# Optimization experiments

Hardware: AMD Instinct MI355X
Metric: run time of the kernel (lower is better)

The kernel has to match this reference:

```python
import jax, jax.numpy as jnp
import numpy as np

EPS = 1e-5

def mvn(x):
    # x: [B, C, H, W]; per-(B,C) mean/std over spatial dims, torch unbiased var
    B, C, H, W = x.shape
    xf = x.reshape(B, C, H * W)
    mean = jnp.mean(xf, axis=2)
    var = jnp.var(xf, axis=2, ddof=1) + EPS
    std = jnp.sqrt(var)
    return (x - mean[:, :, None, None]) / std[:, :, None, None]

def conv1x1(x, w, b):
    # x: [B, Cin, H, W], w: [Cout, Cin], b: [Cout]
    return jnp.einsum('bchw,oc->bohw', x, w) + b[None, :, None, None]

def setup_inputs() -> dict:
    key = jax.random.key(0)
    ks = jax.random.split(key, 10)
    B, V, QK, H, W = 4, 512, 512, 64, 64
    d = {
        'c_x':  jax.random.normal(ks[0], (B, V, H, W), jnp.float32),
        's_x':  jax.random.normal(ks[1], (B, V, H, W), jnp.float32),
        'c_1x': jax.random.normal(ks[2], (B, QK, H, W), jnp.float32),
        's_1x': jax.random.normal(ks[3], (B, QK, H, W), jnp.float32),
        'f_w': jax.random.normal(ks[4], (QK, QK), jnp.float32) * (1.0 / np.sqrt(QK)),
        'f_b': jax.random.normal(ks[5], (QK,), jnp.float32) * 0.01,
        'g_w': jax.random.normal(ks[6], (QK, QK), jnp.float32) * (1.0 / np.sqrt(QK)),
        'g_b': jax.random.normal(ks[7], (QK,), jnp.float32) * 0.01,
        'h_w': jax.random.normal(ks[8], (V, V), jnp.float32) * (1.0 / np.sqrt(V)),
        'h_b': jax.random.normal(ks[9], (V,), jnp.float32) * 0.01,
    }
    return d

def reference(c_x, s_x, c_1x, s_1x, f_w, f_b, g_w, g_b, h_w, h_b):
    B, V, H, W = c_x.shape
    QK = c_1x.shape[1]
    Lq = H * W
    Lk = s_1x.shape[2] * s_1x.shape[3]
    # Q: [B, Lq, QK], K: [B, QK, Lk], V_: [B, Lk, V]
    Q = conv1x1(mvn(c_1x), f_w, f_b).reshape(B, QK, Lq).transpose(0, 2, 1)
    K = conv1x1(mvn(s_1x), g_w, g_b).reshape(B, QK, Lk)
    V_ = conv1x1(s_x, h_w, h_b).reshape(B, V, Lk).transpose(0, 2, 1)
    A = jax.nn.softmax(jnp.einsum('bqc,bck->bqk', Q, K), axis=-1)  # [B, Lq, Lk]
    M = jnp.einsum('bqk,bkv->bqv', A, V_)                          # weighted mean
    Var = jnp.einsum('bqk,bkv->bqv', A, V_ * V_) - M * M           # weighted var
    S = jnp.sqrt(jnp.clip(Var, 0.0, None))
    M = M.transpose(0, 2, 1).reshape(c_x.shape)
    S = S.transpose(0, 2, 1).reshape(c_x.shape)
    return S * mvn(c_x) + M
```

## Files before the change

### kernel.cpp

```cpp
#include <hip/hip_runtime.h>
#include <math.h>

typedef __attribute__((ext_vector_type(8))) short short8;
typedef __attribute__((ext_vector_type(4))) float f32x4;
typedef __attribute__((ext_vector_type(4))) unsigned short u16x4;

#define DEVINL static __device__ __forceinline__
#define MFMA  __builtin_amdgcn_mfma_f32_16x16x32_bf16
#define MFMAH __builtin_amdgcn_mfma_f32_16x16x32_f16

DEVINL unsigned short f2bf(float f){
  union { float f; unsigned u; } v; v.f = f;
  unsigned r = v.u + 0x7FFFu + ((v.u >> 16) & 1u);
  return (unsigned short)(r >> 16);
}
DEVINL float bf2f(unsigned short h){
  union { unsigned u; float f; } v; v.u = ((unsigned)h) << 16;
  return v.f;
}
DEVINL unsigned short f2h(float f){
  union { _Float16 h; unsigned short u; } c; c.h = (_Float16)f;
  return c.u;
}
DEVINL void gload16(const void* g, void* l){
  __builtin_amdgcn_global_load_lds(
      (const __attribute__((address_space(1))) void*)g,
      (__attribute__((address_space(3))) void*)l, 16, 0, 0);
}

__global__ void rowstats_k(const float* __restrict__ x,
                           float* __restrict__ mean, float* __restrict__ rstd){
  int row = blockIdx.x;
  const float4* p = (const float4*)(x + (long)row * 4096);
  float s = 0.f, ss = 0.f;
  for (int i = threadIdx.x; i < 1024; i += 256){
    float4 v = p[i];
    s  += v.x + v.y + v.z + v.w;
    ss += v.x*v.x + v.y*v.y + v.z*v.z + v.w*v.w;
  }
  for (int o = 32; o > 0; o >>= 1){ s += __shfl_down(s, o); ss += __shfl_down(ss, o); }
  __shared__ float ls[4], lss[4];
  int wv = threadIdx.x >> 6;
  if ((threadIdx.x & 63) == 0){ ls[wv] = s; lss[wv] = ss; }
  __syncthreads();
  if (threadIdx.x == 0){
    s = ls[0]+ls[1]+ls[2]+ls[3]; ss = lss[0]+lss[1]+lss[2]+lss[3];
    float m = s * (1.f/4096.f);
    float var = (ss - s*m) * (1.f/4095.f);
    mean[row] = m;
    rstd[row] = 1.f / sqrtf(var + 1e-5f);
  }
}

__global__ void foldw2_k(const float* __restrict__ fw, const float* __restrict__ fb,
                         const float* __restrict__ mQ, const float* __restrict__ rQ,
                         unsigned short* __restrict__ Wfh, unsigned short* __restrict__ Wfl,
                         float* __restrict__ bF,
                         const float* __restrict__ gw, const float* __restrict__ gb,
                         const float* __restrict__ mK, const float* __restrict__ rK,
                         unsigned short* __restrict__ Wgh, unsigned short* __restrict__ Wgl,
                         float* __restrict__ bG){
  int o = blockIdx.x;
  int g = blockIdx.y;
  const float* w    = g ? gw : fw;
  const float* bias = g ? gb : fb;
  const float* mean = g ? mK : mQ;
  const float* rstd = g ? rK : rQ;
  unsigned short* wh = g ? Wgh : Wfh;
  unsigned short* wl = g ? Wgl : Wfl;
  float* biasp = g ? bG : bF;
  const float* wr = w + (long)o * 512;
  float part = 0.f;
  for (int c = threadIdx.x; c < 512; c += 256){
    float wv = wr[c] * rstd[c];
    unsigned short h = f2bf(wv);
    wh[(o<<9)+c] = h;
    wl[(o<<9)+c] = f2bf(wv - bf2f(h));
    part += wv * mean[c];
  }
  __shared__ float red[256];
  red[threadIdx.x] = part; __syncthreads();
  for (int st = 128; st > 0; st >>= 1){
    if (threadIdx.x < st) red[threadIdx.x] += red[threadIdx.x + st];
    __syncthreads();
  }
  if (threadIdx.x == 0) biasp[o] = bias[o] - red[0];
}

__global__ void wsplit_k(const float* __restrict__ w,
                         unsigned short* __restrict__ wh, unsigned short* __restrict__ wl){
  int i = blockIdx.x * 256 + threadIdx.x;
  float v = w[i];
  unsigned short h = f2bf(v);
  wh[i] = h; wl[i] = f2bf(v - bf2f(h));
}

__global__ __launch_bounds__(512) void conv3qk_k(
    const float* __restrict__ X0, const float* __restrict__ X1,
    const unsigned short* __restrict__ Wh0, const unsigned short* __restrict__ Wl0,
    const unsigned short* __restrict__ Wh1, const unsigned short* __restrict__ Wl1,
    const float* __restrict__ b0, const float* __restrict__ b1,
    unsigned short* __restrict__ of0, unsigned short* __restrict__ of1)
{
  int ob = blockIdx.y, lb = blockIdx.x, z = blockIdx.z;
  const float* X = z ? X1 : X0;
  const unsigned short* Wh = z ? Wh1 : Wh0;
  const unsigned short* Wl = z ? Wl1 : Wl0;
  const float* biasp = z ? b1 : b0;
  unsigned short* of = z ? of1 : of0;

  __shared__ __align__(16) char csm[36864];
  typedef unsigned short (*XT)[64][72];
  XT Xh = (XT)csm;
  XT Xl = (XT)(csm + 18432);

  int tid = threadIdx.x, w = tid >> 6, lane = tid & 63, lr = lane & 15, lg = lane >> 4;
  const unsigned short* WhB = Wh + (long)(ob*128 + w*16) * 512;
  const unsigned short* WlB = Wl + (long)(ob*128 + w*16) * 512;
  int sl = tid & 63, scg = tid >> 6;
  const float* Xg = X + (long)(scg*8)*4096 + lb*64 + sl;

  f32x4 acc[4] = {};
  float fA[8], fB[8];
  short8 wA0, wA1, wA2, wA3, wB0, wB1, wB2, wB3;

#define CV_XLOAD(F, CB) { _Pragma("unroll") for (int j=0;j<8;++j) F[j] = Xg[(long)((CB)*64 + j)*4096]; }
#define CV_XWRITE(BUF, F) { short8 hv, lv; _Pragma("unroll") for (int j=0;j<8;++j){ \
    unsigned short h_ = f2bf(F[j]); hv[j] = (short)h_; lv[j] = (short)f2bf(F[j] - bf2f(h_)); } \
    *(short8*)&Xh[BUF][sl][scg*8] = hv; *(short8*)&Xl[BUF][sl][scg*8] = lv; }
#define CV_WLOAD(W0,W1,W2,W3, CB) { \
    W0 = *(const short8*)(WhB + (long)lr*512 + (CB)*64 + lg*8); \
    W1 = *(const short8*)(WhB + (long)lr*512 + (CB)*64 + 32 + lg*8); \
    W2 = *(const short8*)(WlB + (long)lr*512 + (CB)*64 + lg*8); \
    W3 = *(const short8*)(WlB + (long)lr*512 + (CB)*64 + 32 + lg*8); }
#define CV_COMPUTE(BUF, W0,W1,W2,W3) { \
    _Pragma("unroll") for (int ct=0;ct<4;++ct){ \
      short8 bh = *(const short8*)&Xh[BUF][ct*16+lr][lg*8]; \
      short8 bl = *(const short8*)&Xl[BUF][ct*16+lr][lg*8]; \
      acc[ct] = MFMA(W0, bh, acc[ct], 0,0,0); \
      acc[ct] = MFMA(W2, bh, acc[ct], 0,0,0); \
      acc[ct] = MFMA(W0, bl, acc[ct], 0,0,0); } \
    _Pragma("unroll") for (int ct=0;ct<4;++ct){ \
      short8 bh = *(const short8*)&Xh[BUF][ct*16+lr][32+lg*8]; \
      short8 bl = *(const short8*)&Xl[BUF][ct*16+lr][32+lg*8]; \
      acc[ct] = MFMA(W1, bh, acc[ct], 0,0,0); \
      acc[ct] = MFMA(W3, bh, acc[ct], 0,0,0); \
      acc[ct] = MFMA(W1, bl, acc[ct], 0,0,0); } }

  CV_XLOAD(fA, 0); CV_XWRITE(0, fA);
  CV_XLOAD(fA, 1);
  CV_WLOAD(wA0,wA1,wA2,wA3, 0);
  __syncthreads();
  for (int cb = 0; cb < 8; cb += 2){
    if (cb+2 < 8) CV_XLOAD(fB, cb+2);
    CV_WLOAD(wB0,wB1,wB2,wB3, cb+1);
    CV_COMPUTE(0, wA0,wA1,wA2,wA3);
    CV_XWRITE(1, fA);
    __syncthreads();
    if (cb+3 < 8) CV_XLOAD(fA, cb+3);
    if (cb+2 < 8) CV_WLOAD(wA0,wA1,wA2,wA3, cb+2);
    CV_COMPUTE(1, wB0,wB1,wB2,wB3);
    if (cb+2 < 8) CV_XWRITE(0, fB);
    __syncthreads();
  }

  int o4 = ob*128 + w*16 + lg*4;
  float bv[4];
  #pragma unroll
  for (int r = 0; r < 4; ++r) bv[r] = biasp[o4 + r];
  #pragma unroll
  for (int ct = 0; ct < 4; ++ct){
    u16x4 ph;
    #pragma unroll
    for (int r = 0; r < 4; ++r) ph[r] = f2h(acc[ct][r] + bv[r]);
    long base = ((long)(lb*64 + ct*16 + lr)) * 512 + o4;
    *(u16x4*)(of + base) = ph;
  }
}

__global__ __launch_bounds__(512) void conv3v_k(
    const float* __restrict__ X,
    const unsigned short* __restrict__ Wh, const unsigned short* __restrict__ Wl,
    const float* __restrict__ biasp,
    unsigned short* __restrict__ oh,
    unsigned short* __restrict__ o2h, unsigned short* __restrict__ o2l)
{
  int ob = blockIdx.y, lb = blockIdx.x;
  __shared__ __align__(16) char csm[36864];
  typedef unsigned short (*XT)[64][72];
  XT Xh = (XT)csm;
  XT Xl = (XT)(csm + 18432);

  int tid = threadIdx.x, w = tid >> 6, lane = tid & 63, lr = lane & 15, lg = lane >> 4;
  const unsigned short* WhB = Wh + (long)(ob*128 + w*16) * 512;
  const unsigned short* WlB = Wl + (long)(ob*128 + w*16) * 512;
  int sl = tid & 63, scg = tid >> 6;
  const float* Xg = X + (long)(scg*8)*4096 + lb*64 + sl;

  f32x4 acc[4] = {};
  float fA[8], fB[8];
  short8 wA0, wA1, wA2, wA3, wB0, wB1, wB2, wB3;

  CV_XLOAD(fA, 0); CV_XWRITE(0, fA);
  CV_XLOAD(fA, 1);
  CV_WLOAD(wA0,wA1,wA2,wA3, 0);
  __syncthreads();
  for (int cb = 0; cb < 8; cb += 2){
    if (cb+2 < 8) CV_XLOAD(fB, cb+2);
    CV_WLOAD(wB0,wB1,wB2,wB3, cb+1);
    CV_COMPUTE(0, wA0,wA1,wA2,wA3);
    CV_XWRITE(1, fA);
    __syncthreads();
    if (cb+3 < 8) CV_XLOAD(fA, cb+3);
    if (cb+2 < 8) CV_WLOAD(wA0,wA1,wA2,wA3, cb+2);
    CV_COMPUTE(1, wB0,wB1,wB2,wB3);
    if (cb+2 < 8) CV_XWRITE(0, fB);
    __syncthreads();
  }

  int o4 = ob*128 + w*16 + lg*4;
  float bv[4];
  #pragma unroll
  for (int r = 0; r < 4; ++r) bv[r] = biasp[o4 + r];
  unsigned short sh_[16], s2h_[16], s2l_[16];
  #pragma unroll
  for (int ct = 0; ct < 4; ++ct)
    #pragma unroll
    for (int r = 0; r < 4; ++r){
      float y = acc[ct][r] + bv[r];
      unsigned short h = f2bf(y);
      float vhf = bf2f(h);
      float v2 = vhf * vhf;
      unsigned short h2 = f2bf(v2);
      unsigned short l2 = f2bf(v2 - bf2f(h2));
      sh_[ct*4+r] = h; s2h_[ct*4+r] = h2; s2l_[ct*4+r] = l2;
    }
  unsigned short* T = (unsigned short*)csm;
#define CV_STORE(ARR, DST) { \
    __syncthreads(); \
    _Pragma("unroll") for (int ct=0;ct<4;++ct) \
      _Pragma("unroll") for (int r=0;r<4;++r) \
        T[(w*16+lg*4+r)*72 + ct*16+lr] = ARR[ct*4+r]; \
    __syncthreads(); \
    _Pragma("unroll") for (int s_=0;s_<2;++s_){ \
      int slot = tid + s_*512; int row = slot>>3, ch=(slot&7)*8; \
      *(short8*)(DST + (long)(ob*128+row)*4096 + lb*64 + ch) = *(const short8*)&T[row*72+ch]; } }
  CV_STORE(sh_,  oh);
  CV_STORE(s2h_, o2h);
  CV_STORE(s2l_, o2l);
#undef CV_STORE
#undef CV_XLOAD
#undef CV_XWRITE
#undef CV_WLOAD
#undef CV_COMPUTE
}

__global__ __launch_bounds__(512, 4) void sgemm1h_k(
    const unsigned short* __restrict__ Qf, const unsigned short* __restrict__ Kf,
    float* __restrict__ S, int qbase)
{
  int bx = blockIdx.x, by = blockIdx.y;
  int q0g = qbase + bx*128, k0 = by*128;
  __shared__ unsigned short Qs[128][64], Ks[128][64];
  int tid = threadIdx.x, w = tid >> 6, lane = tid & 63, lr = lane & 15, lg = lane >> 4;
  int wr = w & 1, wc = w >> 1;
  int srow = tid >> 3, sch = (tid & 7)*8;
  int swu = ((tid & 7) ^ (srow & 7)) * 8;
  int lr7 = lr & 7;
  short8 qr0, qr1, kr0, kr1;
  f32x4 acc[4][2] = {};

#define SG_LOAD(CB) { long c0_ = (long)(CB)*64 + sch; \
    qr0 = *(const short8*)(Qf + (long)(q0g + srow)*512 + c0_); \
    qr1 = *(const short8*)(Qf + (long)(q0g + srow + 64)*512 + c0_); \
    kr0 = *(const short8*)(Kf + (long)(k0 + srow)*512 + c0_); \
    kr1 = *(const short8*)(Kf + (long)(k0 + srow + 64)*512 + c0_); }
#define SG_WRITE { \
    *(short8*)&Qs[srow][swu] = qr0; *(short8*)&Qs[srow + 64][swu] = qr1; \
    *(short8*)&Ks[srow][swu] = kr0; *(short8*)&Ks[srow + 64][swu] = kr1; }

  SG_LOAD(0); SG_WRITE;
  __syncthreads();
  for (int cb = 0; cb < 8; ++cb){
    if (cb < 7) SG_LOAD(cb+1);
    #pragma unroll
    for (int kk = 0; kk < 2; ++kk){
      int un = ((kk*4 + lg) ^ lr7) * 8;
      short8 bh[2];
      #pragma unroll
      for (int bs = 0; bs < 2; ++bs)
        bh[bs] = *(const short8*)(&Ks[wc*32 + bs*16 + lr][un]);
      #pragma unroll
      for (int as = 0; as < 4; ++as){
        short8 ah = *(const short8*)(&Qs[wr*64 + as*16 + lr][un]);
        #pragma unroll
        for (int bs = 0; bs < 2; ++bs)
          acc[as][bs] = MFMAH(ah, bh[bs], acc[as][bs], 0,0,0);
      }
    }
    __syncthreads();
    if (cb < 7){ SG_WRITE; __syncthreads(); }
  }
#undef SG_LOAD
#undef SG_WRITE
  #pragma unroll
  for (int as = 0; as < 4; ++as){
    #pragma unroll
    for (int bs = 0; bs < 2; ++bs){
      int q = bx*128 + wr*64 + as*16 + lg*4;
      int k = k0 + wc*32 + bs*16 + lr;
      float* Sp = S + (long)q*4096 + k;
      #pragma unroll
      for (int r = 0; r < 4; ++r) Sp[(long)r*4096] = acc[as][bs][r];
    }
  }
}

__global__ __launch_bounds__(256) void softmax_k(const float* __restrict__ S,
                                                 unsigned short* __restrict__ Pb, long pitch,
                                                 int row0, float* __restrict__ inv2){
  int row = blockIdx.x;
  const float* Sr = S + (long)row * 4096;
  int t = threadIdx.x;
  f32x4 v[4];
  #pragma unroll
  for (int i = 0; i < 4; ++i) v[i] = *(const f32x4*)(Sr + t*4 + i*1024);
  float mx = v[0][0];
  #pragma unroll
  for (int i = 0; i < 4; ++i)
    #pragma unroll
    for (int j = 0; j < 4; ++j) mx = fmaxf(mx, v[i][j]);
  #pragma unroll
  for (int o = 32; o > 0; o >>= 1) mx = fmaxf(mx, __shfl_xor(mx, o));
  __shared__ float red[4];
  int wid = t >> 6;
  if ((t & 63) == 0) red[wid] = mx;
  __syncthreads();
  mx = fmaxf(fmaxf(red[0], red[1]), fmaxf(red[2], red[3]));
  __syncthreads();
  float p[16]; float d = 0.f;
  #pragma unroll
  for (int i = 0; i < 4; ++i)
    #pragma unroll
    for (int j = 0; j < 4; ++j){ float e = expf(v[i][j] - mx); p[i*4+j] = e; d += e; }
  #pragma unroll
  for (int o = 32; o > 0; o >>= 1) d += __shfl_xor(d, o);
  if ((t & 63) == 0) red[wid] = d;
  __syncthreads();
  d = red[0] + red[1] + red[2] + red[3];
  __syncthreads();
  float invd = 1.f / d;
  unsigned short pb[16]; float d2 = 0.f;
  #pragma unroll
  for (int i = 0; i < 16; ++i){ pb[i] = f2bf(p[i] * invd); d2 += bf2f(pb[i]); }
  #pragma unroll
  for (int o = 32; o > 0; o >>= 1) d2 += __shfl_xor(d2, o);
  if ((t & 63) == 0) red[wid] = d2;
  __syncthreads();
  if (t == 0) inv2[row0 + row] = 1.f / (red[0]+red[1]+red[2]+red[3]);
  unsigned short* Pr = Pb + (long)(row0 + row) * pitch;
  #pragma unroll
  for (int i = 0; i < 4; ++i){
    u16x4 pk;
    #pragma unroll
    for (int j = 0; j < 4; ++j) pk[j] = pb[i*4+j];
    *(u16x4*)(Pr + t*4 + i*1024) = pk;
  }
}

__global__ __launch_bounds__(256, 2) void pv2_k(
    const unsigned short* __restrict__ P, long ppitch,
    const unsigned short* __restrict__ vh,
    const unsigned short* __restrict__ v2h, const unsigned short* __restrict__ v2l,
    const float* __restrict__ inv2,
    const float* __restrict__ cx, const float* __restrict__ mcx, const float* __restrict__ rcx,
    float* __restrict__ outb, int qP_base, int qG_base)
{
  __shared__ __align__(16) char smem[65536];
  typedef unsigned short (*PlT)[64][64];
  typedef unsigned short (*VlT)[3][64][64];
  PlT Pl = (PlT)smem;
  VlT Vl = (VlT)(smem + 16384);
  float* R = (float*)smem;

  int tid = threadIdx.x;
  int l = tid & 63, w = tid >> 6;
  int wq = w >> 1, wv = w & 1;
  int lr = l & 15, lg = l >> 4;
  int qP0 = qP_base + blockIdx.x*64, qG0 = qG_base + blockIdx.x*64;
  int vc0 = blockIdx.y*64;

  int r8_ = l >> 3, c8 = (l & 7)*8;
  int srcc = c8 ^ (r8_*8);
  const unsigned short* gsrc;
  long rs8;
  unsigned short *l0, *l1;
  if (w == 0){
    gsrc = P + (long)(qP0 + r8_)*ppitch + srcc;
    rs8 = (long)8*ppitch;
    l0 = &Pl[0][0][0]; l1 = &Pl[1][0][0];
  } else {
    const unsigned short* va = (w==1 ? vh : w==2 ? v2h : v2l);
    gsrc = va + (long)(vc0 + r8_)*4096 + srcc;
    rs8 = (long)8*4096;
    l0 = &Vl[0][w-1][0][0]; l1 = &Vl[1][w-1][0][0];
  }

  f32x4 accM[2][2] = {}, acc2[2][2] = {};

#define PV_STAGE(LB, TT) { long ko_ = (long)(TT)*64; \
    _Pragma("unroll") for (int j = 0; j < 8; ++j) \
      gload16(gsrc + j*rs8 + ko_, LB + j*512); }
#define PV_COMPUTE(BUF) { \
    _Pragma("unroll") for (int kk = 0; kk < 2; ++kk){ \
      int un = ((kk*4 + lg) ^ (lr & 7)) * 8; \
      short8 fh[2], f2h[2], f2l[2]; \
      _Pragma("unroll") for (int bs = 0; bs < 2; ++bs){ \
        int vrow = wv*32 + bs*16 + lr; \
        fh[bs]  = *(const short8*)(&Vl[BUF][0][vrow][un]); \
        f2h[bs] = *(const short8*)(&Vl[BUF][1][vrow][un]); \
        f2l[bs] = *(const short8*)(&Vl[BUF][2][vrow][un]); } \
      _Pragma("unroll") for (int aq = 0; aq < 2; ++aq){ \
        short8 pa = *(const short8*)(&Pl[BUF][wq*32 + aq*16 + lr][un]); \
        _Pragma("unroll") for (int bs = 0; bs < 2; ++bs){ \
          accM[aq][bs] = MFMA(pa, fh[bs],  accM[aq][bs], 0,0,0); \
          acc2[aq][bs] = MFMA(pa, f2h[bs], acc2[aq][bs], 0,0,0); \
          acc2[aq][bs] = MFMA(pa, f2l[bs], acc2[aq][bs], 0,0,0); } } } }

  PV_STAGE(l0, 0);
  __syncthreads();
  for (int t = 0; t < 64; ++t){
    unsigned short* nb = (t & 1) ? l0 : l1;
    if (t < 63) PV_STAGE(nb, t+1);
    int buf = t & 1;
    PV_COMPUTE(buf);
    __syncthreads();
  }
#undef PV_STAGE
#undef PV_COMPUTE

  float* Tm = R;
  #pragma unroll
  for (int aq = 0; aq < 2; ++aq)
    #pragma unroll
    for (int bs = 0; bs < 2; ++bs){
      int vcl = wv*32 + bs*16 + lr;
      int ql  = wq*32 + aq*16 + lg*4;
      #pragma unroll
      for (int r = 0; r < 4; ++r) Tm[vcl*68 + ql + r] = accM[aq][bs][r];
    }
  __syncthreads();
  f32x4 Mv[4];
  #pragma unroll
  for (int p = 0; p < 4; ++p){
    int chunk = tid + p*256;
    int row = chunk >> 4, c4 = (chunk & 15)*4;
    Mv[p] = *(const f32x4*)&Tm[row*68 + c4];
  }
  __syncthreads();
  #pragma unroll
  for (int aq = 0; aq < 2; ++aq)
    #pragma unroll
    for (int bs = 0; bs < 2; ++bs){
      int vcl = wv*32 + bs*16 + lr;
      int ql  = wq*32 + aq*16 + lg*4;
      #pragma unroll
      for (int r = 0; r < 4; ++r) Tm[vcl*68 + ql + r] = acc2[aq][bs][r];
    }
  __syncthreads();
  #pragma unroll
  for (int p = 0; p < 4; ++p){
    int chunk = tid + p*256;
    int row = chunk >> 4, c4 = (chunk & 15)*4;
    float mu = mcx[vc0 + row], rs = rcx[vc0 + row];
    f32x4 t2 = *(const f32x4*)&Tm[row*68 + c4];
    f32x4 iv = *(const f32x4*)&inv2[qP0 + c4];
    f32x4 cv = *(const f32x4*)&cx[(long)(vc0+row)*4096 + qG0 + c4];
    f32x4 ov;
    #pragma unroll
    for (int j = 0; j < 4; ++j){
      float M = Mv[p][j]*iv[j], M2 = t2[j]*iv[j];
      float var = M2 - M*M;
      float sd = sqrtf(fmaxf(var, 0.f));
      ov[j] = sd*(cv[j]-mu)*rs + M;
    }
    *(f32x4*)&outb[(long)(vc0+row)*4096 + qG0 + c4] = ov;
  }
}

extern "C" void kernel_launch(void* const* d_in, const int* in_sizes, int n_in,
                              void* d_out, int out_size, void* d_ws, size_t ws_size,
                              hipStream_t stream){
  const float* c_x  = (const float*)d_in[0];
  const float* s_x  = (const float*)d_in[1];
  const float* c_1x = (const float*)d_in[2];
  const float* s_1x = (const float*)d_in[3];
  const float* f_w  = (const float*)d_in[4];
  const float* f_b  = (const float*)d_in[5];
  const float* g_w  = (const float*)d_in[6];
  const float* g_b  = (const float*)d_in[7];
  const float* h_w  = (const float*)d_in[8];
  const float* h_b  = (const float*)d_in[9];
  float* out = (float*)d_out;

  char* ws = (char*)d_ws;
  size_t off = 0;
  auto alloc = [&](size_t bytes)->void*{
    void* p = ws + off; off += (bytes + 255) & ~(size_t)255; return p;
  };
  float* meanQ = (float*)alloc(2048*4); float* rstdQ = (float*)alloc(2048*4);
  float* meanK = (float*)alloc(2048*4); float* rstdK = (float*)alloc(2048*4);
  float* meanC = (float*)alloc(2048*4); float* rstdC = (float*)alloc(2048*4);
  float* biasF = (float*)alloc(512*4);  float* biasG = (float*)alloc(512*4);
  unsigned short* Wfh = (unsigned short*)alloc((size_t)512*512*2);
  unsigned short* Wfl = (unsigned short*)alloc((size_t)512*512*2);
  unsigned short* Wgh = (unsigned short*)alloc((size_t)512*512*2);
  unsigned short* Wgl = (unsigned short*)alloc((size_t)512*512*2);
  unsigned short* Whh = (unsigned short*)alloc((size_t)512*512*2);
  unsigned short* Whl = (unsigned short*)alloc((size_t)512*512*2);
  unsigned short* Qf = (unsigned short*)alloc((size_t)4096*512*2);
  unsigned short* Kf = (unsigned short*)alloc((size_t)4096*512*2);
  unsigned short* vh  = (unsigned short*)alloc((size_t)512*4096*2);
  unsigned short* v2h = (unsigned short*)alloc((size_t)512*4096*2);
  unsigned short* v2l = (unsigned short*)alloc((size_t)512*4096*2);
  float* S    = (float*)alloc((size_t)2048*4096*4);
  float* inv2 = (float*)alloc(4096*4);

  size_t pbytes = (size_t)4096*4096*2;
  bool bigP = (off + pbytes + 256 <= ws_size);
  unsigned short* Pb; long ppitch;
  if (bigP){ Pb = (unsigned short*)alloc(pbytes); ppitch = 4096; }
  else     { Pb = (unsigned short*)S;             ppitch = 8192; }

  rowstats_k<<<2048, 256, 0, stream>>>(c_1x, meanQ, rstdQ);
  rowstats_k<<<2048, 256, 0, stream>>>(s_1x, meanK, rstdK);
  rowstats_k<<<2048, 256, 0, stream>>>(c_x,  meanC, rstdC);
  wsplit_k<<<1024, 256, 0, stream>>>(h_w, Whh, Whl);

  for (int b = 0; b < 4; ++b){
    long xoff = (long)b * 512 * 4096;
    foldw2_k<<<dim3(512,2), 256, 0, stream>>>(f_w, f_b, meanQ + b*512, rstdQ + b*512, Wfh, Wfl, biasF,
                                              g_w, g_b, meanK + b*512, rstdK + b*512, Wgh, Wgl, biasG);
    conv3qk_k<<<dim3(64,4,2), 512, 0, stream>>>(c_1x + xoff, s_1x + xoff,
                                                Wfh, Wfl, Wgh, Wgl, biasF, biasG,
                                                Qf, Kf);
    conv3v_k<<<dim3(64,4), 512, 0, stream>>>(s_x + xoff, Whh, Whl, h_b, vh, v2h, v2l);
    if (bigP){
      for (int ch = 0; ch < 2; ++ch){
        int qbase = ch * 2048;
        sgemm1h_k<<<dim3(16,32), 512, 0, stream>>>(Qf, Kf, S, qbase);
        softmax_k<<<2048, 256, 0, stream>>>(S, Pb, 4096, qbase, inv2);
      }
      pv2_k<<<dim3(64,8), 256, 0, stream>>>(Pb, 4096, vh, v2h, v2l, inv2,
                                            c_x + xoff, meanC + b*512, rstdC + b*512,
                                            out + xoff, 0, 0);
    } else {
      for (int ch = 0; ch < 2; ++ch){
        int qbase = ch * 2048;
        sgemm1h_k<<<dim3(16,32), 512, 0, stream>>>(Qf, Kf, S, qbase);
        softmax_k<<<2048, 256, 0, stream>>>(S, Pb, 8192, 0, inv2);
        pv2_k<<<dim3(32,8), 256, 0, stream>>>(Pb, 8192, vh, v2h, v2l, inv2,
                                              c_x + xoff, meanC + b*512, rstdC + b*512,
                                              out + xoff, 0, qbase);
      }
    }
  }
}
```

Before: 635.1 us.

## Store attention scores in fp16 and softmax in place over full query range

The score GEMM now writes fp16 scores instead of fp32, and softmax overwrites that same buffer with bf16 probabilities. This halves score traffic and drops the separate probability buffer. With the smaller buffer, all 4096 queries run in one pass, collapsing the two-chunk launch sequence into single sgemm/softmax/pv launches per batch. The cost is precision: logits are rounded to fp16 before exp, which may hurt accuracy or overflow for large scores.

Result: faster. 575.4 us (-9.4%).

```diff
diff --git a/kernel.cpp b/kernel.cpp
--- a/kernel.cpp
+++ b/kernel.cpp
@@ -21,6 +21,10 @@
 DEVINL unsigned short f2h(float f){
   union { _Float16 h; unsigned short u; } c; c.h = (_Float16)f;
   return c.u;
+}
+DEVINL float h2f(unsigned short u){
+  union { unsigned short u; _Float16 h; } c; c.u = u;
+  return (float)c.h;
 }
 DEVINL void gload16(const void* g, void* l){
   __builtin_amdgcn_global_load_lds(
@@ -257,10 +261,10 @@
 
 __global__ __launch_bounds__(512, 4) void sgemm1h_k(
     const unsigned short* __restrict__ Qf, const unsigned short* __restrict__ Kf,
-    float* __restrict__ S, int qbase)
+    unsigned short* __restrict__ S)
 {
   int bx = blockIdx.x, by = blockIdx.y;
-  int q0g = qbase + bx*128, k0 = by*128;
+  int q0g = bx*128, k0 = by*128;
   __shared__ unsigned short Qs[128][64], Ks[128][64];
   int tid = threadIdx.x, w = tid >> 6, lane = tid & 63, lr = lane & 15, lg = lane >> 4;
   int wr = w & 1, wc = w >> 1;
@@ -307,29 +311,28 @@
   for (int as = 0; as < 4; ++as){
     #pragma unroll
     for (int bs = 0; bs < 2; ++bs){
-      int q = bx*128 + wr*64 + as*16 + lg*4;
+      int q = q0g + wr*64 + as*16 + lg*4;
       int k = k0 + wc*32 + bs*16 + lr;
-      float* Sp = S + (long)q*4096 + k;
+      unsigned short* Sp = S + (long)q*4096 + k;
       #pragma unroll
-      for (int r = 0; r < 4; ++r) Sp[(long)r*4096] = acc[as][bs][r];
+      for (int r = 0; r < 4; ++r) Sp[(long)r*4096] = f2h(acc[as][bs][r]);
     }
   }
 }
 
-__global__ __launch_bounds__(256) void softmax_k(const float* __restrict__ S,
-                                                 unsigned short* __restrict__ Pb, long pitch,
-                                                 int row0, float* __restrict__ inv2){
+__global__ __launch_bounds__(256) void softmax_k(unsigned short* __restrict__ SP,
+                                                 float* __restrict__ inv2){
   int row = blockIdx.x;
-  const float* Sr = S + (long)row * 4096;
+  unsigned short* Sr = SP + (long)row * 4096;
   int t = threadIdx.x;
-  f32x4 v[4];
-  #pragma unroll
-  for (int i = 0; i < 4; ++i) v[i] = *(const f32x4*)(Sr + t*4 + i*1024);
-  float mx = v[0][0];
-  #pragma unroll
-  for (int i = 0; i < 4; ++i)
-    #pragma unroll
-    for (int j = 0; j < 4; ++j) mx = fmaxf(mx, v[i][j]);
+  short8 a = *(const short8*)(Sr + t*8);
+  short8 b = *(const short8*)(Sr + 2048 + t*8);
+  float v[16];
+  #pragma unroll
+  for (int j = 0; j < 8; ++j){ v[j] = h2f((unsigned short)a[j]); v[8+j] = h2f((unsigned short)b[j]); }
+  float mx = v[0];
+  #pragma unroll
+  for (int i = 1; i < 16; ++i) mx = fmaxf(mx, v[i]);
   #pragma unroll
   for (int o = 32; o > 0; o >>= 1) mx = fmaxf(mx, __shfl_xor(mx, o));
   __shared__ float red[4];
@@ -340,9 +343,7 @@
   __syncthreads();
   float p[16]; float d = 0.f;
   #pragma unroll
-  for (int i = 0; i < 4; ++i)
-    #pragma unroll
-    for (int j = 0; j < 4; ++j){ float e = expf(v[i][j] - mx); p[i*4+j] = e; d += e; }
+  for (int i = 0; i < 16; ++i){ float e = expf(v[i] - mx); p[i] = e; d += e; }
   #pragma unroll
   for (int o = 32; o > 0; o >>= 1) d += __shfl_xor(d, o);
   if ((t & 63) == 0) red[wid] = d;
@@ -357,15 +358,12 @@
   for (int o = 32; o > 0; o >>= 1) d2 += __shfl_xor(d2, o);
   if ((t & 63) == 0) red[wid] = d2;
   __syncthreads();
-  if (t == 0) inv2[row0 + row] = 1.f / (red[0]+red[1]+red[2]+red[3]);
-  unsigned short* Pr = Pb + (long)(row0 + row) * pitch;
-  #pragma unroll
-  for (int i = 0; i < 4; ++i){
-    u16x4 pk;
-    #pragma unroll
-    for (int j = 0; j < 4; ++j) pk[j] = pb[i*4+j];
-    *(u16x4*)(Pr + t*4 + i*1024) = pk;
-  }
+  if (t == 0) inv2[row] = 1.f / (red[0]+red[1]+red[2]+red[3]);
+  short8 pa, pbv;
+  #pragma unroll
+  for (int j = 0; j < 8; ++j){ pa[j] = (short)pb[j]; pbv[j] = (short)pb[8+j]; }
+  *(short8*)(Sr + t*8) = pa;
+  *(short8*)(Sr + 2048 + t*8) = pbv;
 }
 
 __global__ __launch_bounds__(256, 2) void pv2_k(
@@ -374,7 +372,7 @@
     const unsigned short* __restrict__ v2h, const unsigned short* __restrict__ v2l,
     const float* __restrict__ inv2,
     const float* __restrict__ cx, const float* __restrict__ mcx, const float* __restrict__ rcx,
-    float* __restrict__ outb, int qP_base, int qG_base)
+    float* __restrict__ outb)
 {
   __shared__ __align__(16) char smem[65536];
   typedef unsigned short (*PlT)[64][64];
@@ -387,7 +385,7 @@
   int l = tid & 63, w = tid >> 6;
   int wq = w >> 1, wv = w & 1;
   int lr = l & 15, lg = l >> 4;
-  int qP0 = qP_base + blockIdx.x*64, qG0 = qG_base + blockIdx.x*64;
+  int qP0 = blockIdx.x*64, qG0 = blockIdx.x*64;
   int vc0 = blockIdx.y*64;
 
   int r8_ = l >> 3, c8 = (l & 7)*8;
@@ -414,18 +412,18 @@
 #define PV_COMPUTE(BUF) { \
     _Pragma("unroll") for (int kk = 0; kk < 2; ++kk){ \
       int un = ((kk*4 + lg) ^ (lr & 7)) * 8; \
-      short8 fh[2], f2h[2], f2l[2]; \
+      short8 fh[2], f2h_[2], f2l_[2]; \
       _Pragma("unroll") for (int bs = 0; bs < 2; ++bs){ \
         int vrow = wv*32 + bs*16 + lr; \
-        fh[bs]  = *(const short8*)(&Vl[BUF][0][vrow][un]); \
-        f2h[bs] = *(const short8*)(&Vl[BUF][1][vrow][un]); \
-        f2l[bs] = *(const short8*)(&Vl[BUF][2][vrow][un]); } \
+        fh[bs]   = *(const short8*)(&Vl[BUF][0][vrow][un]); \
+        f2h_[bs] = *(const short8*)(&Vl[BUF][1][vrow][un]); \
+        f2l_[bs] = *(const short8*)(&Vl[BUF][2][vrow][un]); } \
       _Pragma("unroll") for (int aq = 0; aq < 2; ++aq){ \
         short8 pa = *(const short8*)(&Pl[BUF][wq*32 + aq*16 + lr][un]); \
         _Pragma("unroll") for (int bs = 0; bs < 2; ++bs){ \
-          accM[aq][bs] = MFMA(pa, fh[bs],  accM[aq][bs], 0,0,0); \
-          acc2[aq][bs] = MFMA(pa, f2h[bs], acc2[aq][bs], 0,0,0); \
-          acc2[aq][bs] = MFMA(pa, f2l[bs], acc2[aq][bs], 0,0,0); } } } }
+          accM[aq][bs] = MFMA(pa, fh[bs],   accM[aq][bs], 0,0,0); \
+          acc2[aq][bs] = MFMA(pa, f2h_[bs], acc2[aq][bs], 0,0,0); \
+          acc2[aq][bs] = MFMA(pa, f2l_[bs], acc2[aq][bs], 0,0,0); } } } }
 
   PV_STAGE(l0, 0);
   __syncthreads();
@@ -523,14 +521,8 @@
   unsigned short* vh  = (unsigned short*)alloc((size_t)512*4096*2);
   unsigned short* v2h = (unsigned short*)alloc((size_t)512*4096*2);
   unsigned short* v2l = (unsigned short*)alloc((size_t)512*4096*2);
-  float* S    = (float*)alloc((size_t)2048*4096*4);
+  unsigned short* S   = (unsigned short*)alloc((size_t)4096*4096*2);
   float* inv2 = (float*)alloc(4096*4);
-
-  size_t pbytes = (size_t)4096*4096*2;
-  bool bigP = (off + pbytes + 256 <= ws_size);
-  unsigned short* Pb; long ppitch;
-  if (bigP){ Pb = (unsigned short*)alloc(pbytes); ppitch = 4096; }
-  else     { Pb = (unsigned short*)S;             ppitch = 8192; }
 
   rowstats_k<<<2048, 256, 0, stream>>>(c_1x, meanQ, rstdQ);
   rowstats_k<<<2048, 256, 0, stream>>>(s_1x, meanK, rstdK);
@@ -545,24 +537,10 @@
                                                 Wfh, Wfl, Wgh, Wgl, biasF, biasG,
                                                 Qf, Kf);
     conv3v_k<<<dim3(64,4), 512, 0, stream>>>(s_x + xoff, Whh, Whl, h_b, vh, v2h, v2l);
-    if (bigP){
-      for (int ch = 0; ch < 2; ++ch){
-        int qbase = ch * 2048;
-        sgemm1h_k<<<dim3(16,32), 512, 0, stream>>>(Qf, Kf, S, qbase);
-        softmax_k<<<2048, 256, 0, stream>>>(S, Pb, 4096, qbase, inv2);
-      }
-      pv2_k<<<dim3(64,8), 256, 0, stream>>>(Pb, 4096, vh, v2h, v2l, inv2,
-                                            c_x + xoff, meanC + b*512, rstdC + b*512,
-                                            out + xoff, 0, 0);
-    } else {
-      for (int ch = 0; ch < 2; ++ch){
-        int qbase = ch * 2048;
-        sgemm1h_k<<<dim3(16,32), 512, 0, stream>>>(Qf, Kf, S, qbase);
-        softmax_k<<<2048, 256, 0, stream>>>(S, Pb, 8192, 0, inv2);
-        pv2_k<<<dim3(32,8), 256, 0, stream>>>(Pb, 8192, vh, v2h, v2l, inv2,
-                                              c_x + xoff, meanC + b*512, rstdC + b*512,
-                                              out + xoff, 0, qbase);
-      }
-    }
-  }
-}
+    sgemm1h_k<<<dim3(32,32), 512, 0, stream>>>(Qf, Kf, S);
+    softmax_k<<<4096, 256, 0, stream>>>(S, inv2);
+    pv2_k<<<dim3(64,8), 256, 0, stream>>>(S, 4096, vh, v2h, v2l, inv2,
+                                          c_x + xoff, meanC + b*512, rstdC + b*512,
+                                          out + xoff);
+  }
+}
```
